# Optimization experiments

Hardware: AMD Instinct MI355X
Metric: run time of the kernel (lower is better)

Reference implementation:

```python
import jax, jax.numpy as jnp
import numpy as np

SMALL_NUMBER = 1e-07
N, C, H, D = 100000, 128, 128, 3  # nodes, input_size, hidden_size, spatial dim


def _glorot(key, shape):
    r = np.sqrt(6.0 / (shape[-2] + shape[-1]))
    return jax.random.uniform(key, shape, dtype=jnp.float32, minval=-r, maxval=r)


def setup_inputs() -> dict:
    key = jax.random.key(0)
    ks = jax.random.split(key, 12)
    return {
        "v": jax.random.normal(ks[0], (N, C, D), dtype=jnp.float32),
        "m_v": jax.random.normal(ks[1], (N, H, D), dtype=jnp.float32),
        "Wh_z": _glorot(ks[2], (H, C)),
        "Wi_z": _glorot(ks[3], (C, C)),
        "b_z": jnp.zeros((1, C), dtype=jnp.float32),
        "Wh_r": _glorot(ks[4], (H, C)),
        "Wi_r": _glorot(ks[5], (C, C)),
        "b_r": jnp.zeros((1, C), dtype=jnp.float32),
        "Wh_v": _glorot(ks[6], (H, C)),
        "Wi_v": _glorot(ks[7], (C, C)),
        "Wq": _glorot(ks[8], (C, C)),
        "Wk": _glorot(ks[9], (C, C)),
    }


def _vlin(x, w):
    # x: [N, C_in, D], w: [C_in, C_out] -> [N, C_out, D]
    return jnp.einsum('ncd,co->nod', x, w)


def _vn_leaky(x, Wq, Wk, alpha=0.3):
    # x: [N, C, D]
    Q = jnp.einsum('ncd,cq->nqd', x, Wq)  # [N, C, D]
    K = jnp.einsum('ncd,ck->nkd', x, Wk)  # [N, C, D]
    inner = jnp.einsum('ncd,ncd->nc', Q, K)           # [N, C]
    inner = jnp.minimum(inner, 0.0)[:, :, None]        # inner * (inner < 0)
    k_norm = jnp.linalg.norm(K, axis=-1)[:, :, None] + SMALL_NUMBER  # [N, C, 1]
    out = Q - inner * K / jnp.square(k_norm)
    return alpha * x + (1.0 - alpha) * out


def reference(v, m_v, Wh_z, Wi_z, b_z, Wh_r, Wi_r, b_r, Wh_v, Wi_v, Wq, Wk):
    z = _vlin(m_v, Wh_z) + _vlin(v, Wi_z)                       # [N, C, D]
    z = jax.nn.sigmoid(jnp.linalg.norm(z, axis=-1) + b_z)[:, :, None]  # [N, C, 1]
    r = _vlin(m_v, Wh_r) + _vlin(v, Wi_r)
    r = jax.nn.sigmoid(jnp.linalg.norm(r, axis=-1) + b_r)[:, :, None]
    delta_v = _vlin(m_v, Wh_v) + _vlin(r * v, Wi_v)
    delta_v = _vn_leaky(delta_v, Wq, Wk)
    return (1.0 - z) * v + z * delta_v
```

## Files before the change

### kernel.cpp

```cpp
#include <hip/hip_runtime.h>


#define NN   100000
#define NT   16
#define NBLK (NN / NT)
#define PSZ  16384
#define FS   520
#define TSZ  (12 * FS)
#define GAP  32

typedef unsigned short us;
typedef us     us8    __attribute__((ext_vector_type(8)));
typedef __bf16 bf16x8 __attribute__((ext_vector_type(8)));
typedef float  f32x4  __attribute__((ext_vector_type(4)));

#define MFMA __builtin_amdgcn_mfma_f32_16x16x32_bf16

__device__ __forceinline__ us f2b(float f) {
    union { float f; unsigned u; } x; x.f = f;
    return (us)((x.u + 0x7FFFu + ((x.u >> 16) & 1u)) >> 16);
}
__device__ __forceinline__ float b2f(us h) {
    union { unsigned u; float f; } x; x.u = ((unsigned)h) << 16;
    return x.f;
}

__global__ void prep_weights(const float* __restrict__ Whz, const float* __restrict__ Wiz,
                             const float* __restrict__ Whr, const float* __restrict__ Wir,
                             const float* __restrict__ Whv, const float* __restrict__ Wiv,
                             const float* __restrict__ Wq,  const float* __restrict__ Wk,
                             us* __restrict__ ws) {
    const int mid = blockIdx.x >> 3;
    const int s = ((blockIdx.x & 7) << 8) + threadIdx.x;
    const float* W; int hp, lp;
    switch (mid) {
        case 0: W = Whz; hp = 0;  lp = -1; break;
        case 1: W = Wiz; hp = 1;  lp = -1; break;
        case 2: W = Whr; hp = 2;  lp = 3;  break;
        case 3: W = Wir; hp = 4;  lp = 5;  break;
        case 4: W = Whv; hp = 6;  lp = 7;  break;
        case 5: W = Wiv; hp = 8;  lp = 9;  break;
        case 6: W = Wq;  hp = 10; lp = -1; break;
        default: W = Wk; hp = 11; lp = 12; break;
    }
    const int f = s >> 6, l = s & 63;
    const int o  = (f >> 2) * 16 + (l & 15);
    const int c0 = (f & 3) * 32 + (l >> 4) * 8;
    us8 hi, lo;
#pragma unroll
    for (int j = 0; j < 8; ++j) {
        float x = W[(c0 + j) * 128 + o];
        us h = f2b(x);
        hi[j] = h;
        lo[j] = f2b(x - b2f(h));
    }
    *(us8*)(ws + hp * PSZ + s * 8) = hi;
    if (lp >= 0) *(us8*)(ws + lp * PSZ + s * 8) = lo;
}

__device__ __forceinline__ void loadB4(const us* __restrict__ p, int wb, bf16x8* d) {
#pragma unroll
    for (int kf = 0; kf < 4; ++kf) d[kf] = *(const bf16x8*)(p + wb + kf * 512);
}

__device__ __forceinline__ void mm_zr(const us* __restrict__ Ah, const us* __restrict__ Al,
                                      const bf16x8* bz, const bf16x8* bh, const bf16x8* bl,
                                      f32x4* zacc, f32x4* racc, int ab) {
#pragma unroll
    for (int kf = 0; kf < 4; ++kf)
#pragma unroll
        for (int m = 0; m < 3; ++m) {
            bf16x8 ah = *(const bf16x8*)(Ah + (m * 4 + kf) * FS + ab);
            bf16x8 al = *(const bf16x8*)(Al + (m * 4 + kf) * FS + ab);
            zacc[m] = MFMA(ah, bz[kf], zacc[m], 0, 0, 0);
            racc[m] = MFMA(ah, bh[kf], racc[m], 0, 0, 0);
            racc[m] = MFMA(al, bh[kf], racc[m], 0, 0, 0);
            racc[m] = MFMA(ah, bl[kf], racc[m], 0, 0, 0);
        }
}
__device__ __forceinline__ void mm_s(const us* __restrict__ Ah, const us* __restrict__ Al,
                                     const bf16x8* bh, const bf16x8* bl,
                                     f32x4* acc, int ab) {
#pragma unroll
    for (int kf = 0; kf < 4; ++kf)
#pragma unroll
        for (int m = 0; m < 3; ++m) {
            bf16x8 ah = *(const bf16x8*)(Ah + (m * 4 + kf) * FS + ab);
            bf16x8 al = *(const bf16x8*)(Al + (m * 4 + kf) * FS + ab);
            acc[m] = MFMA(ah, bh[kf], acc[m], 0, 0, 0);
            acc[m] = MFMA(al, bh[kf], acc[m], 0, 0, 0);
            acc[m] = MFMA(ah, bl[kf], acc[m], 0, 0, 0);
        }
}
__device__ __forceinline__ void mm_qk(const us* __restrict__ Dh, const us* __restrict__ Dl,
                                      const bf16x8* bq, const bf16x8* bh, const bf16x8* bl,
                                      f32x4* qacc, f32x4* kacc, int ab) {
#pragma unroll
    for (int kf = 0; kf < 4; ++kf)
#pragma unroll
        for (int m = 0; m < 3; ++m) {
            bf16x8 dh = *(const bf16x8*)(Dh + (m * 4 + kf) * FS + ab);
            bf16x8 dl = *(const bf16x8*)(Dl + (m * 4 + kf) * FS + ab);
            qacc[m] = MFMA(dh, bq[kf], qacc[m], 0, 0, 0);
            kacc[m] = MFMA(dh, bh[kf], kacc[m], 0, 0, 0);
            kacc[m] = MFMA(dl, bh[kf], kacc[m], 0, 0, 0);
            kacc[m] = MFMA(dh, bl[kf], kacc[m], 0, 0, 0);
        }
}

__global__ __launch_bounds__(512, 4) void gru_vn_fused(
    const float* __restrict__ v, const float* __restrict__ mv,
    const float* __restrict__ bz, const float* __restrict__ br,
    const us* __restrict__ ws, float* __restrict__ out)
{
    __shared__ __align__(16) us pool[4 * TSZ + GAP];
    __shared__ __align__(16) float r_t[128 * 17];

    us* const vth = pool;
    us* const vtl = pool + TSZ;
    us* const mvh = pool + 2 * TSZ + GAP;
    us* const mvl = pool + 3 * TSZ + GAP;

    const int tid  = threadIdx.x;
    const int lane = tid & 63;
    const int wave = tid >> 6;
    const int arow = lane & 15;
    const int bo   = wave * 16 + arow;
    const int rsub = (lane >> 4) * 4;
    const int ab   = lane * 8;
    const int wb   = wave * 2048 + lane * 8;
    const int n0   = blockIdx.x * NT;

    const us* pWhz  = ws;            const us* pWiz  = ws + 1 * PSZ;
    const us* pWhrh = ws + 2 * PSZ;  const us* pWhrl = ws + 3 * PSZ;
    const us* pWirh = ws + 4 * PSZ;  const us* pWirl = ws + 5 * PSZ;
    const us* pWhvh = ws + 6 * PSZ;  const us* pWhvl = ws + 7 * PSZ;
    const us* pWivh = ws + 8 * PSZ;  const us* pWivl = ws + 9 * PSZ;
    const us* pWq   = ws + 10 * PSZ; const us* pWkh  = ws + 11 * PSZ;
    const us* pWkl  = ws + 12 * PSZ;

    {
        const int which = tid & 1;
        const int c8    = (tid >> 1) & 15;
        const int ind   = tid >> 5;
        const float* src = (which ? mv : v) + (size_t)(n0 + ind) * 384 + c8 * 24;
        float x[24];
#pragma unroll
        for (int t = 0; t < 6; ++t) *(float4*)(x + 4 * t) = *(const float4*)(src + 4 * t);
        us* const dh = which ? mvh : vth;
        us* const dl = which ? mvl : vtl;
        const int f0  = c8 >> 2;
        const int row = ind + ((c8 & 3) << 4);
#pragma unroll
        for (int d = 0; d < 3; ++d) {
            us8 hh, ll;
#pragma unroll
            for (int j = 0; j < 8; ++j) {
                float xv = x[j * 3 + d];
                __bf16 h = (__bf16)xv;
                hh[j] = __builtin_bit_cast(us, h);
                ll[j] = __builtin_bit_cast(us, (__bf16)(xv - (float)h));
            }
            const int off = (d * 4 + f0) * FS + row * 8;
            *(us8*)(dh + off) = hh;
            *(us8*)(dl + off) = ll;
        }
    }
    const float bzv = bz[bo], brv = br[bo];
    const f32x4 Z4 = {0.f, 0.f, 0.f, 0.f};

    bf16x8 Bz[4], Brh[4], Brl[4];
    loadB4(pWhz, wb, Bz); loadB4(pWhrh, wb, Brh); loadB4(pWhrl, wb, Brl);
    __syncthreads();

    f32x4 zacc[3] = {Z4, Z4, Z4}, racc[3] = {Z4, Z4, Z4};
    mm_zr(mvh, mvl, Bz, Brh, Brl, zacc, racc, ab);
    loadB4(pWiz, wb, Bz); loadB4(pWirh, wb, Brh); loadB4(pWirl, wb, Brl);
    mm_zr(vth, vtl, Bz, Brh, Brl, zacc, racc, ab);

    const int vbase = (bo >> 5) * FS + (rsub + (((bo >> 3) & 3) << 4)) * 8 + (bo & 7);
    float zz[4], vout[4][3];
#pragma unroll
    for (int q = 0; q < 4; ++q) {
        float h0 = zacc[0][q], h1 = zacc[1][q], h2 = zacc[2][q];
        zz[q] = 1.f / (1.f + __expf(-(sqrtf(h0 * h0 + h1 * h1 + h2 * h2) + bzv)));
        float r0 = racc[0][q], r1 = racc[1][q], r2 = racc[2][q];
        float rr = 1.f / (1.f + __expf(-(sqrtf(r0 * r0 + r1 * r1 + r2 * r2) + brv)));
        r_t[bo * 17 + rsub + q] = rr;
#pragma unroll
        for (int d = 0; d < 3; ++d) {
            int off = vbase + d * 4 * FS + q * 8;
            vout[q][d] = b2f(vth[off]) + b2f(vtl[off]);
        }
    }
    bf16x8 Bdh[4], Bdl[4];
    loadB4(pWhvh, wb, Bdh); loadB4(pWhvl, wb, Bdl);
    __syncthreads();

#pragma unroll
    for (int it = 0; it < 2; ++it) {
        int s = tid + it * 512;
        if (s < 768) {
            int f = s >> 6, l = s & 63;
            int i = l & 15, cb = ((f & 3) << 5) + ((l >> 4) << 3);
            int off = f * FS + l * 8;
            us8 vh8 = *(const us8*)(vth + off);
            us8 vl8 = *(const us8*)(vtl + off);
            us8 oh, ol;
#pragma unroll
            for (int j = 0; j < 8; ++j) {
                float p = r_t[(cb + j) * 17 + i] * (b2f(vh8[j]) + b2f(vl8[j]));
                __bf16 h = (__bf16)p;
                oh[j] = __builtin_bit_cast(us, h);
                ol[j] = __builtin_bit_cast(us, (__bf16)(p - (float)h));
            }
            *(us8*)(vth + off) = oh;
            *(us8*)(vtl + off) = ol;
        }
    }
    __syncthreads();

    f32x4 dacc[3] = {Z4, Z4, Z4};
    mm_s(mvh, mvl, Bdh, Bdl, dacc, ab);
    loadB4(pWivh, wb, Bdh); loadB4(pWivl, wb, Bdl);
    mm_s(vth, vtl, Bdh, Bdl, dacc, ab);
    __syncthreads();

#pragma unroll
    for (int m = 0; m < 3; ++m)
#pragma unroll
    for (int q = 0; q < 4; ++q) {
        int off = vbase + m * 4 * FS + q * 8;
        float x = dacc[m][q];
        __bf16 h = (__bf16)x;
        mvh[off] = __builtin_bit_cast(us, h);
        mvl[off] = __builtin_bit_cast(us, (__bf16)(x - (float)h));
    }
    bf16x8 Bq[4], Bkh[4], Bkl[4];
    loadB4(pWq, wb, Bq); loadB4(pWkh, wb, Bkh); loadB4(pWkl, wb, Bkl);
    __syncthreads();

    f32x4 qacc[3] = {Z4, Z4, Z4}, kacc[3] = {Z4, Z4, Z4};
    mm_qk(mvh, mvl, Bq, Bkh, Bkl, qacc, kacc, ab);

#pragma unroll
    for (int q = 0; q < 4; ++q) {
        const int i = rsub + q;
        float q0 = qacc[0][q], q1 = qacc[1][q], q2 = qacc[2][q];
        float k0 = kacc[0][q], k1 = kacc[1][q], k2 = kacc[2][q];
        float inner = fminf(q0 * k0 + q1 * k1 + q2 * k2, 0.f);
        float kn = sqrtf(k0 * k0 + k1 * k1 + k2 * k2) + 1e-7f;
        float s = inner / (kn * kn);
        float z = zz[q];
        float dv0 = 0.3f * dacc[0][q] + 0.7f * (q0 - s * k0);
        float dv1 = 0.3f * dacc[1][q] + 0.7f * (q1 - s * k1);
        float dv2 = 0.3f * dacc[2][q] + 0.7f * (q2 - s * k2);
        float* op = out + ((size_t)(n0 + i) * 128 + bo) * 3;
        op[0] = (1.f - z) * vout[q][0] + z * dv0;
        op[1] = (1.f - z) * vout[q][1] + z * dv1;
        op[2] = (1.f - z) * vout[q][2] + z * dv2;
    }
}

extern "C" void kernel_launch(void* const* d_in, const int* in_sizes, int n_in,
                              void* d_out, int out_size, void* d_ws, size_t ws_size,
                              hipStream_t stream) {
    (void)in_sizes; (void)n_in; (void)ws_size; (void)out_size;
    us* ws = (us*)d_ws;
    prep_weights<<<64, 256, 0, stream>>>(
        (const float*)d_in[2],  (const float*)d_in[3],
        (const float*)d_in[5],  (const float*)d_in[6],
        (const float*)d_in[8],  (const float*)d_in[9],
        (const float*)d_in[10], (const float*)d_in[11], ws);
    gru_vn_fused<<<NBLK, 512, 0, stream>>>(
        (const float*)d_in[0], (const float*)d_in[1],
        (const float*)d_in[4], (const float*)d_in[7],
        ws, (float*)d_out);
}
```

Baseline: 242.7 us.

## Precompose Wh_v/Wi_v with Wq/Wk to compute delta, Q, K in one pass

```diff
diff --git a/kernel.cpp b/kernel.cpp
--- a/kernel.cpp
+++ b/kernel.cpp
@@ -28,20 +28,17 @@
 __global__ void prep_weights(const float* __restrict__ Whz, const float* __restrict__ Wiz,
                              const float* __restrict__ Whr, const float* __restrict__ Wir,
                              const float* __restrict__ Whv, const float* __restrict__ Wiv,
-                             const float* __restrict__ Wq,  const float* __restrict__ Wk,
                              us* __restrict__ ws) {
     const int mid = blockIdx.x >> 3;
     const int s = ((blockIdx.x & 7) << 8) + threadIdx.x;
     const float* W; int hp, lp;
     switch (mid) {
-        case 0: W = Whz; hp = 0;  lp = -1; break;
-        case 1: W = Wiz; hp = 1;  lp = -1; break;
-        case 2: W = Whr; hp = 2;  lp = 3;  break;
-        case 3: W = Wir; hp = 4;  lp = 5;  break;
-        case 4: W = Whv; hp = 6;  lp = 7;  break;
-        case 5: W = Wiv; hp = 8;  lp = 9;  break;
-        case 6: W = Wq;  hp = 10; lp = -1; break;
-        default: W = Wk; hp = 11; lp = 12; break;
+        case 0: W = Whz; hp = 0; lp = -1; break;
+        case 1: W = Wiz; hp = 1; lp = -1; break;
+        case 2: W = Whr; hp = 2; lp = 3;  break;
+        case 3: W = Wir; hp = 4; lp = 5;  break;
+        case 4: W = Whv; hp = 6; lp = 7;  break;
+        default: W = Wiv; hp = 8; lp = 9; break;
     }
     const int f = s >> 6, l = s & 63;
     const int o  = (f >> 2) * 16 + (l & 15);
@@ -58,11 +55,72 @@
     if (lp >= 0) *(us8*)(ws + lp * PSZ + s * 8) = lo;
 }
 
+__global__ void prep_comp(const float* __restrict__ Whv, const float* __restrict__ Wiv,
+                          const float* __restrict__ Wq,  const float* __restrict__ Wk,
+                          us* __restrict__ ws) {
+    __shared__ float arow[128];
+    const int mat = blockIdx.x >> 7;
+    const int c   = blockIdx.x & 127;
+    const int o   = threadIdx.x;
+    const float* A = (mat & 1) ? Wiv : Whv;
+    const float* B = (mat & 2) ? Wk  : Wq;
+    arow[o] = A[c * 128 + o];
+    __syncthreads();
+    float a0 = 0.f, a1 = 0.f, a2 = 0.f, a3 = 0.f;
+#pragma unroll 8
+    for (int k = 0; k < 128; k += 4) {
+        a0 += arow[k + 0] * B[(k + 0) * 128 + o];
+        a1 += arow[k + 1] * B[(k + 1) * 128 + o];
+        a2 += arow[k + 2] * B[(k + 2) * 128 + o];
+        a3 += arow[k + 3] * B[(k + 3) * 128 + o];
+    }
+    float t = (a0 + a1) + (a2 + a3);
+    const int f = (o >> 4) * 4 + (c >> 5);
+    const int l = (((c >> 3) & 3) << 4) + (o & 15);
+    const int off = (f * 64 + l) * 8 + (c & 7);
+    const int hp = (mat & 2) ? (10 + (mat & 1) * 0 + 2 + (mat & 1) * 2) : (10 + (mat & 1));
+    us h = f2b(t);
+    ws[hp * PSZ + off] = h;
+    if (mat & 2) ws[(hp + 1) * PSZ + off] = f2b(t - b2f(h));
+}
+
+__device__ __forceinline__ void p2_load(const us* __restrict__ ws, int wb, int kf, bf16x8* B) {
+#pragma unroll
+    for (int j = 0; j < 10; ++j)
+        B[j] = *(const bf16x8*)(ws + (6 + j) * PSZ + wb + kf * 512);
+}
+__device__ __forceinline__ void p2_step(const us* __restrict__ mvh, const us* __restrict__ mvl,
+                                        const us* __restrict__ vth, const us* __restrict__ vtl,
+                                        const bf16x8* B, int kf, int ab,
+                                        f32x4* dacc, f32x4* qacc, f32x4* kacc) {
+#pragma unroll
+    for (int m = 0; m < 3; ++m) {
+        const int fo = (m * 4 + kf) * FS + ab;
+        bf16x8 ah = *(const bf16x8*)(mvh + fo);
+        bf16x8 al = *(const bf16x8*)(mvl + fo);
+        dacc[m] = MFMA(ah, B[0], dacc[m], 0, 0, 0);
+        dacc[m] = MFMA(al, B[0], dacc[m], 0, 0, 0);
+        dacc[m] = MFMA(ah, B[1], dacc[m], 0, 0, 0);
+        qacc[m] = MFMA(ah, B[4], qacc[m], 0, 0, 0);
+        kacc[m] = MFMA(ah, B[6], kacc[m], 0, 0, 0);
+        kacc[m] = MFMA(al, B[6], kacc[m], 0, 0, 0);
+        kacc[m] = MFMA(ah, B[7], kacc[m], 0, 0, 0);
+        bf16x8 rh = *(const bf16x8*)(vth + fo);
+        bf16x8 rl = *(const bf16x8*)(vtl + fo);
+        dacc[m] = MFMA(rh, B[2], dacc[m], 0, 0, 0);
+        dacc[m] = MFMA(rl, B[2], dacc[m], 0, 0, 0);
+        dacc[m] = MFMA(rh, B[3], dacc[m], 0, 0, 0);
+        qacc[m] = MFMA(rh, B[5], qacc[m], 0, 0, 0);
+        kacc[m] = MFMA(rh, B[8], kacc[m], 0, 0, 0);
+        kacc[m] = MFMA(rl, B[8], kacc[m], 0, 0, 0);
+        kacc[m] = MFMA(rh, B[9], kacc[m], 0, 0, 0);
+    }
+}
+
 __device__ __forceinline__ void loadB4(const us* __restrict__ p, int wb, bf16x8* d) {
 #pragma unroll
     for (int kf = 0; kf < 4; ++kf) d[kf] = *(const bf16x8*)(p + wb + kf * 512);
 }
-
 __device__ __forceinline__ void mm_zr(const us* __restrict__ Ah, const us* __restrict__ Al,
                                       const bf16x8* bz, const bf16x8* bh, const bf16x8* bl,
                                       f32x4* zacc, f32x4* racc, int ab) {
@@ -76,35 +134,6 @@
             racc[m] = MFMA(ah, bh[kf], racc[m], 0, 0, 0);
             racc[m] = MFMA(al, bh[kf], racc[m], 0, 0, 0);
             racc[m] = MFMA(ah, bl[kf], racc[m], 0, 0, 0);
-        }
-}
-__device__ __forceinline__ void mm_s(const us* __restrict__ Ah, const us* __restrict__ Al,
-                                     const bf16x8* bh, const bf16x8* bl,
-                                     f32x4* acc, int ab) {
-#pragma unroll
-    for (int kf = 0; kf < 4; ++kf)
-#pragma unroll
-        for (int m = 0; m < 3; ++m) {
-            bf16x8 ah = *(const bf16x8*)(Ah + (m * 4 + kf) * FS + ab);
-            bf16x8 al = *(const bf16x8*)(Al + (m * 4 + kf) * FS + ab);
-            acc[m] = MFMA(ah, bh[kf], acc[m], 0, 0, 0);
-            acc[m] = MFMA(al, bh[kf], acc[m], 0, 0, 0);
-            acc[m] = MFMA(ah, bl[kf], acc[m], 0, 0, 0);
-        }
-}
-__device__ __forceinline__ void mm_qk(const us* __restrict__ Dh, const us* __restrict__ Dl,
-                                      const bf16x8* bq, const bf16x8* bh, const bf16x8* bl,
-                                      f32x4* qacc, f32x4* kacc, int ab) {
-#pragma unroll
-    for (int kf = 0; kf < 4; ++kf)
-#pragma unroll
-        for (int m = 0; m < 3; ++m) {
-            bf16x8 dh = *(const bf16x8*)(Dh + (m * 4 + kf) * FS + ab);
-            bf16x8 dl = *(const bf16x8*)(Dl + (m * 4 + kf) * FS + ab);
-            qacc[m] = MFMA(dh, bq[kf], qacc[m], 0, 0, 0);
-            kacc[m] = MFMA(dh, bh[kf], kacc[m], 0, 0, 0);
-            kacc[m] = MFMA(dl, bh[kf], kacc[m], 0, 0, 0);
-            kacc[m] = MFMA(dh, bl[kf], kacc[m], 0, 0, 0);
         }
 }
 
@@ -134,10 +163,6 @@
     const us* pWhz  = ws;            const us* pWiz  = ws + 1 * PSZ;
     const us* pWhrh = ws + 2 * PSZ;  const us* pWhrl = ws + 3 * PSZ;
     const us* pWirh = ws + 4 * PSZ;  const us* pWirl = ws + 5 * PSZ;
-    const us* pWhvh = ws + 6 * PSZ;  const us* pWhvl = ws + 7 * PSZ;
-    const us* pWivh = ws + 8 * PSZ;  const us* pWivl = ws + 9 * PSZ;
-    const us* pWq   = ws + 10 * PSZ; const us* pWkh  = ws + 11 * PSZ;
-    const us* pWkl  = ws + 12 * PSZ;
 
     {
         const int which = tid & 1;
@@ -193,8 +218,8 @@
             vout[q][d] = b2f(vth[off]) + b2f(vtl[off]);
         }
     }
-    bf16x8 Bdh[4], Bdl[4];
-    loadB4(pWhvh, wb, Bdh); loadB4(pWhvl, wb, Bdl);
+    bf16x8 B0[10];
+    p2_load(ws, wb, 0, B0);
     __syncthreads();
 
 #pragma unroll
@@ -220,28 +245,14 @@
     }
     __syncthreads();
 
-    f32x4 dacc[3] = {Z4, Z4, Z4};
-    mm_s(mvh, mvl, Bdh, Bdl, dacc, ab);
-    loadB4(pWivh, wb, Bdh); loadB4(pWivl, wb, Bdl);
-    mm_s(vth, vtl, Bdh, Bdl, dacc, ab);
-    __syncthreads();
-
-#pragma unroll
-    for (int m = 0; m < 3; ++m)
-#pragma unroll
-    for (int q = 0; q < 4; ++q) {
-        int off = vbase + m * 4 * FS + q * 8;
-        float x = dacc[m][q];
-        __bf16 h = (__bf16)x;
-        mvh[off] = __builtin_bit_cast(us, h);
-        mvl[off] = __builtin_bit_cast(us, (__bf16)(x - (float)h));
-    }
-    bf16x8 Bq[4], Bkh[4], Bkl[4];
-    loadB4(pWq, wb, Bq); loadB4(pWkh, wb, Bkh); loadB4(pWkl, wb, Bkl);
-    __syncthreads();
-
-    f32x4 qacc[3] = {Z4, Z4, Z4}, kacc[3] = {Z4, Z4, Z4};
-    mm_qk(mvh, mvl, Bq, Bkh, Bkl, qacc, kacc, ab);
+    f32x4 dacc[3] = {Z4, Z4, Z4}, qacc[3] = {Z4, Z4, Z4}, kacc[3] = {Z4, Z4, Z4};
+    p2_step(mvh, mvl, vth, vtl, B0, 0, ab, dacc, qacc, kacc);
+#pragma unroll
+    for (int kf = 1; kf < 4; ++kf) {
+        bf16x8 B[10];
+        p2_load(ws, wb, kf, B);
+        p2_step(mvh, mvl, vth, vtl, B, kf, ab, dacc, qacc, kacc);
+    }
 
 #pragma unroll
     for (int q = 0; q < 4; ++q) {
@@ -267,9 +278,11 @@
                               hipStream_t stream) {
     (void)in_sizes; (void)n_in; (void)ws_size; (void)out_size;
     us* ws = (us*)d_ws;
-    prep_weights<<<64, 256, 0, stream>>>(
-        (const float*)d_in[2],  (const float*)d_in[3],
-        (const float*)d_in[5],  (const float*)d_in[6],
+    prep_weights<<<48, 256, 0, stream>>>(
+        (const float*)d_in[2], (const float*)d_in[3],
+        (const float*)d_in[5], (const float*)d_in[6],
+        (const float*)d_in[8], (const float*)d_in[9], ws);
+    prep_comp<<<512, 128, 0, stream>>>(
         (const float*)d_in[8],  (const float*)d_in[9],
         (const float*)d_in[10], (const float*)d_in[11], ws);
     gru_vn_fused<<<NBLK, 512, 0, stream>>>(
```

After: 312.1 us. 1.29x slower.
